# Performance work log

Hardware: AMD Instinct MI355X
Metric: run time of the kernel (lower is better)

## Reference

```python
import jax, jax.numpy as jnp
import numpy as np
from functools import partial

EPS = 1e-5
TAU = 0.1

def bn(x, g, b, axes):
    m = jnp.mean(x, axis=axes, keepdims=True)
    v = jnp.var(x, axis=axes, keepdims=True)
    return (x - m) * jax.lax.rsqrt(v + EPS) * g + b

def conv(x, w, b):
    # x: NCHW, w: OIHW, stride 1, padding 1
    y = jax.lax.conv_general_dilated(x, w, (1, 1), ((1, 1), (1, 1)),
                                     dimension_numbers=('NCHW', 'OIHW', 'NCHW'))
    return y + b[None, :, None, None]

def maxpool2(x):
    return jax.lax.reduce_window(x, -jnp.inf, jax.lax.max, (1, 1, 2, 2), (1, 1, 2, 2), 'VALID')

def setup_inputs() -> dict:
    key = jax.random.key(0)
    ks = jax.random.split(key, 24)
    s = 0.02
    B = 4096
    d = {}
    d['input_data'] = jax.random.normal(ks[0], (B, 3, 32, 32), jnp.float32)
    d['conv1_w'] = jax.random.normal(ks[1], (32, 3, 3, 3), jnp.float32) * s
    d['conv1_b'] = jnp.zeros((32,), jnp.float32)
    d['bn1_g'] = jnp.ones((32,), jnp.float32); d['bn1_b'] = jnp.zeros((32,), jnp.float32)
    d['conv2_w'] = jax.random.normal(ks[2], (64, 32, 3, 3), jnp.float32) * s
    d['conv2_b'] = jnp.zeros((64,), jnp.float32)
    d['bn2_g'] = jnp.ones((64,), jnp.float32); d['bn2_b'] = jnp.zeros((64,), jnp.float32)
    d['conv3_w'] = jax.random.normal(ks[3], (128, 64, 3, 3), jnp.float32) * s
    d['conv3_b'] = jnp.zeros((128,), jnp.float32)
    d['bn3_g'] = jnp.ones((128,), jnp.float32); d['bn3_b'] = jnp.zeros((128,), jnp.float32)
    d['pre_w'] = jax.random.normal(ks[4], (1024, 8192), jnp.float32) * s
    d['pre_b'] = jnp.zeros((1024,), jnp.float32)
    d['bnp_g'] = jnp.ones((1024,), jnp.float32); d['bnp_b'] = jnp.zeros((1024,), jnp.float32)
    d['disc_w'] = jax.random.normal(ks[5], (384, 1024), jnp.float32) * s
    d['disc_b'] = jnp.zeros((384,), jnp.float32)
    d['bnd_g'] = jnp.ones((384,), jnp.float32); d['bnd_b'] = jnp.zeros((384,), jnp.float32)
    d['dfc_w'] = jax.random.normal(ks[6], (2, 384), jnp.float32) * s
    d['dfc_b'] = jnp.zeros((2,), jnp.float32)
    d['sw_w'] = jax.random.normal(ks[7], (2, 384), jnp.float32) * s
    d['sw_b'] = jnp.zeros((2,), jnp.float32)
    # partitioned classifier: P=2, Linear(1024 -> 192) + ReLU + Linear(192 -> 10)
    d['p1_w'] = jax.random.normal(ks[8], (2, 192, 1024), jnp.float32) * s
    d['p1_b'] = jnp.zeros((2, 192), jnp.float32)
    d['p2_w'] = jax.random.normal(ks[9], (2, 10, 192), jnp.float32) * s
    d['p2_b'] = jnp.zeros((2, 10), jnp.float32)
    return d

def reference(input_data, conv1_w, conv1_b, bn1_g, bn1_b, conv2_w, conv2_b, bn2_g, bn2_b,
              conv3_w, conv3_b, bn3_g, bn3_b, pre_w, pre_b, bnp_g, bnp_b,
              disc_w, disc_b, bnd_g, bnd_b, dfc_w, dfc_b, sw_w, sw_b,
              p1_w, p1_b, p2_w, p2_b):
    B = input_data.shape[0]
    # feature extractor
    x = jax.nn.relu(bn(conv(input_data, conv1_w, conv1_b), bn1_g[None, :, None, None], bn1_b[None, :, None, None], (0, 2, 3)))
    x = maxpool2(x)
    x = jax.nn.relu(bn(conv(x, conv2_w, conv2_b), bn2_g[None, :, None, None], bn2_b[None, :, None, None], (0, 2, 3)))
    x = maxpool2(x)
    x = jax.nn.relu(bn(conv(x, conv3_w, conv3_b), bn3_g[None, :, None, None], bn3_b[None, :, None, None], (0, 2, 3)))
    feat = x.reshape(B, -1)  # [B, 8192]
    feat = jax.nn.relu(bn(feat @ pre_w.T + pre_b, bnp_g[None, :], bnp_b[None, :], (0,)))  # [B, 1024]
    # discriminator branch
    dpen = jax.nn.relu(bn(feat @ disc_w.T + disc_b, bnd_g[None, :], bnd_b[None, :], (0,)))  # [B, 384]
    domain_output = dpen @ dfc_w.T + dfc_b  # [B, 2]
    sw_logits = dpen @ sw_w.T + sw_b  # [B, P]
    # gumbel-softmax (soft) + multinomial sample of partition
    key = jax.random.key(42)
    k1, k2 = jax.random.split(key)
    u = jax.random.uniform(k1, sw_logits.shape, jnp.float32, 1e-10, 1.0)
    gumbel = -jnp.log(-jnp.log(u))
    y = jax.nn.softmax((sw_logits + gumbel) / TAU, axis=-1)  # [B, P]
    partition_idx = jax.random.categorical(k2, jnp.log(y + 1e-20), axis=-1)  # [B]
    # per-partition expert MLP computed densely (P=2), then gather chosen partition
    h = jax.nn.relu(jnp.einsum('bi,poi->pbo', feat, p1_w) + p1_b[:, None, :])  # [P, B, 192]
    logits = jnp.einsum('pbo,pco->pbc', h, p2_w) + p2_b[:, None, :]  # [P, B, 10]
    sel = logits[partition_idx, jnp.arange(B)]  # [B, 10]
    # original multiplies single-element stack by full gumbel vector and sums -> scale by sum(y)=1
    class_output_partitioned = sel * jnp.sum(y, axis=1, keepdims=True)
    return (class_output_partitioned, domain_output, partition_idx)
```

## Files before the change

### kernel.cpp

```cpp
#include <hip/hip_runtime.h>
#include <cstdint>
#include <cstddef>

typedef __attribute__((ext_vector_type(8))) short short8;
typedef __attribute__((ext_vector_type(4))) float f32x4;

__host__ __device__ inline void threefry2x32(uint32_t k0, uint32_t k1,
                                             uint32_t x0, uint32_t x1,
                                             uint32_t& o0, uint32_t& o1) {
  uint32_t ks2 = k0 ^ k1 ^ 0x1BD11BDAu;
  uint32_t v0 = x0 + k0, v1 = x1 + k1;
#define TF_R(r) { v0 += v1; v1 = (v1 << (r)) | (v1 >> (32 - (r))); v1 ^= v0; }
  TF_R(13) TF_R(15) TF_R(26) TF_R(6)
  v0 += k1; v1 += ks2 + 1u;
  TF_R(17) TF_R(29) TF_R(16) TF_R(24)
  v0 += ks2; v1 += k0 + 2u;
  TF_R(13) TF_R(15) TF_R(26) TF_R(6)
  v0 += k0; v1 += k1 + 3u;
  TF_R(17) TF_R(29) TF_R(16) TF_R(24)
  v0 += k1; v1 += ks2 + 4u;
  TF_R(13) TF_R(15) TF_R(26) TF_R(6)
  v0 += ks2; v1 += k0 + 5u;
#undef TF_R
  o0 = v0; o1 = v1;
}

__device__ __forceinline__ uint32_t tf_bits32(uint32_t k0, uint32_t k1, uint32_t j) {
  uint32_t o0, o1;
  threefry2x32(k0, k1, 0u, j, o0, o1);
  return o0 ^ o1;
}

__device__ __forceinline__ float u01_from_bits(uint32_t bits) {
  return __uint_as_float((bits >> 9) | 0x3f800000u) - 1.0f;
}

__device__ __forceinline__ float waveSum(float v) {
#pragma unroll
  for (int off = 32; off > 0; off >>= 1) v += __shfl_down(v, off, 64);
  return v;
}

__global__ __launch_bounds__(256) void conv1_fused_kernel(
    const float* __restrict__ in, const float* __restrict__ w,
    float* __restrict__ outraw, float* __restrict__ partials) {
  __shared__ float ins[3 * 34 * 34];
  __shared__ float red[4][64];
  const int b = blockIdx.x, t = threadIdx.x;
  for (int i = t; i < 3 * 34 * 34; i += 256) {
    int ci = i / 1156, r = i % 1156, iy = r / 34, ix = r % 34;
    int y = iy - 1, x = ix - 1;
    float v = 0.f;
    if ((unsigned)y < 32u && (unsigned)x < 32u)
      v = in[(((size_t)b * 3 + ci) * 32 + y) * 32 + x];
    ins[i] = v;
  }
  __syncthreads();
  const int py = t >> 4, px = t & 15, wv = t >> 6, ln = t & 63;
  float win[3][4][4];
#pragma unroll
  for (int ci = 0; ci < 3; ci++)
#pragma unroll
    for (int r = 0; r < 4; r++)
#pragma unroll
      for (int c = 0; c < 4; c++)
        win[ci][r][c] = ins[ci * 1156 + (2 * py + r) * 34 + (2 * px + c)];
#pragma unroll 1
  for (int co = 0; co < 32; co++) {
    float acc00 = 0.f, acc01 = 0.f, acc10 = 0.f, acc11 = 0.f;
#pragma unroll
    for (int ci = 0; ci < 3; ci++) {
      const float* wp = w + (co * 3 + ci) * 9;
#pragma unroll
      for (int dy = 0; dy < 3; dy++)
#pragma unroll
        for (int dx = 0; dx < 3; dx++) {
          float wvv = wp[dy * 3 + dx];
          acc00 += win[ci][dy][dx] * wvv;
          acc01 += win[ci][dy][dx + 1] * wvv;
          acc10 += win[ci][dy + 1][dx] * wvv;
          acc11 += win[ci][dy + 1][dx + 1] * wvv;
        }
    }
    float sm = acc00 + acc01 + acc10 + acc11;
    float sq = acc00 * acc00 + acc01 * acc01 + acc10 * acc10 + acc11 * acc11;
    float s = waveSum(sm), q = waveSum(sq);
    if (ln == 0) { red[wv][2 * co] = s; red[wv][2 * co + 1] = q; }
    float m = fmaxf(fmaxf(acc00, acc01), fmaxf(acc10, acc11));
    outraw[(((size_t)b * 32 + co) * 16 + py) * 16 + px] = m;
  }
  __syncthreads();
  for (int i = t; i < 64; i += 256)
    partials[(size_t)b * 64 + i] = red[0][i] + red[1][i] + red[2][i] + red[3][i];
}

__device__ __forceinline__ uint32_t pack_bf16q(float x) {
  uint32_t u = __float_as_uint(x);
  uint32_t hi = (u + 0x7fffu + ((u >> 16) & 1u)) & 0xffff0000u;
  float r = x - __uint_as_float(hi);
  uint32_t v = __float_as_uint(r);
  uint32_t lo = (v + 0x7fffu + ((v >> 16) & 1u)) >> 16;
  return hi | lo;
}

__global__ void cvt_bf16q_kernel(const float* X, uint32_t* Y, int n4) {
  int i = blockIdx.x * blockDim.x + threadIdx.x;
  if (i >= n4) return;
  float4 x = ((const float4*)X)[i];
  uint4 o;
  o.x = pack_bf16q(x.x); o.y = pack_bf16q(x.y);
  o.z = pack_bf16q(x.z); o.w = pack_bf16q(x.w);
  ((uint4*)Y)[i] = o;
}

__global__ void prep_w2_kernel(const float* __restrict__ w, short* __restrict__ wh,
                               short* __restrict__ wl) {
  int idx = blockIdx.x * 256 + threadIdx.x;
  if (idx >= 64 * 32 * 9) return;
  int tp = idx % 9, rem = idx / 9;
  int ci = rem % 32, co = rem / 32;
  uint32_t pq = pack_bf16q(w[idx]);
  size_t o = ((size_t)tp * 64 + co) * 32 + ci;
  wh[o] = (short)(pq >> 16);
  wl[o] = (short)(pq & 0xffffu);
}

__global__ void prep_w3_kernel(const float* __restrict__ w, short* __restrict__ wh,
                               short* __restrict__ wl) {
  int idx = blockIdx.x * 256 + threadIdx.x;
  if (idx >= 128 * 64 * 9) return;
  int tp = idx % 9, rem = idx / 9;
  int ci = rem % 64, co = rem / 64;
  uint32_t pq = pack_bf16q(w[idx]);
  size_t o = ((size_t)tp * 128 + co) * 64 + ci;
  wh[o] = (short)(pq >> 16);
  wl[o] = (short)(pq & 0xffffu);
}

__global__ __launch_bounds__(256) void conv2_mfma_kernel(
    const uint32_t* __restrict__ inq, const short* __restrict__ wh,
    const short* __restrict__ wl, float* __restrict__ outpool,
    float* __restrict__ partials) {
  __shared__ short Xh[324 * 32], Xl[324 * 32];
  __shared__ float red[4][128];
  const int b = blockIdx.x, t = threadIdx.x;
  for (int i = t; i < 324 * 16; i += 256) {
    int row = i >> 4;
    int py = row / 18, pxx = row % 18;
    if (py == 0 || py == 17 || pxx == 0 || pxx == 17) {
      ((uint32_t*)Xh)[i] = 0u;
      ((uint32_t*)Xl)[i] = 0u;
    }
  }
  for (int i = t; i < 4096; i += 256) {
    int p = i >> 8, px = i & 255;
    int y = px >> 4, x = px & 15;
    uint32_t ua = inq[((size_t)b * 32 + 2 * p) * 256 + px];
    uint32_t ub = inq[((size_t)b * 32 + 2 * p + 1) * 256 + px];
    uint32_t h = (ua >> 16) | (ub & 0xffff0000u);
    uint32_t l = (ua & 0xffffu) | (ub << 16);
    int row = (y + 1) * 18 + (x + 1);
    int ci2 = (2 * p) ^ ((row & 3) << 3);
    ((uint32_t*)Xh)[(row * 32 + ci2) >> 1] = h;
    ((uint32_t*)Xl)[(row * 32 + ci2) >> 1] = l;
  }
  __syncthreads();
  const int w = t >> 6, l = t & 63;
  const int lr = l & 15, lg = l >> 4;
  f32x4 acc[4][4];
#pragma unroll
  for (int i = 0; i < 4; i++)
#pragma unroll
    for (int j = 0; j < 4; j++) acc[i][j] = (f32x4){0.f, 0.f, 0.f, 0.f};
#pragma unroll 1
  for (int tap = 0; tap < 9; tap++) {
    const int dy = tap / 3, dx = tap % 3;
    short8 awh[4], awl[4];
#pragma unroll
    for (int i = 0; i < 4; i++) {
      size_t off = ((size_t)tap * 64 + i * 16 + lr) * 32 + lg * 8;
      awh[i] = *(const short8*)(wh + off);
      awl[i] = *(const short8*)(wl + off);
    }
    short8 bxh[4], bxl[4];
#pragma unroll
    for (int j = 0; j < 4; j++) {
      int y = w * 4 + j, x = lr;
      int row = (y + dy) * 18 + (x + dx);
      int ci = (lg * 8) ^ ((row & 3) << 3);
      bxh[j] = *(const short8*)&Xh[row * 32 + ci];
      bxl[j] = *(const short8*)&Xl[row * 32 + ci];
    }
#pragma unroll
    for (int i = 0; i < 4; i++)
#pragma unroll
      for (int j = 0; j < 4; j++) {
        acc[i][j] = __builtin_amdgcn_mfma_f32_16x16x32_bf16(awh[i], bxh[j], acc[i][j], 0, 0, 0);
        acc[i][j] = __builtin_amdgcn_mfma_f32_16x16x32_bf16(awh[i], bxl[j], acc[i][j], 0, 0, 0);
        acc[i][j] = __builtin_amdgcn_mfma_f32_16x16x32_bf16(awl[i], bxh[j], acc[i][j], 0, 0, 0);
      }
  }
#pragma unroll
  for (int i = 0; i < 4; i++)
#pragma unroll
    for (int r = 0; r < 4; r++) {
      int co = i * 16 + lg * 4 + r;
      float v0 = acc[i][0][r], v1 = acc[i][1][r], v2 = acc[i][2][r], v3 = acc[i][3][r];
      float s = v0 + v1 + v2 + v3;
      float q = v0 * v0 + v1 * v1 + v2 * v2 + v3 * v3;
#pragma unroll
      for (int off = 1; off <= 8; off <<= 1) {
        s += __shfl_xor(s, off, 64);
        q += __shfl_xor(q, off, 64);
      }
      if (lr == 0) { red[w][2 * co] = s; red[w][2 * co + 1] = q; }
      float h0 = fmaxf(v0, __shfl_xor(v0, 1, 64));
      float h1 = fmaxf(v1, __shfl_xor(v1, 1, 64));
      float h2 = fmaxf(v2, __shfl_xor(v2, 1, 64));
      float h3 = fmaxf(v3, __shfl_xor(v3, 1, 64));
      float pm0 = fmaxf(h0, h1);
      float pm1 = fmaxf(h2, h3);
      if ((lr & 1) == 0) {
        size_t base = ((size_t)b * 64 + co) * 64 + (w * 2) * 8 + (lr >> 1);
        outpool[base] = pm0;
        outpool[base + 8] = pm1;
      }
    }
  __syncthreads();
  for (int i = t; i < 128; i += 256)
    partials[(size_t)b * 128 + i] = red[0][i] + red[1][i] + red[2][i] + red[3][i];
}

__global__ __launch_bounds__(256) void conv3_mfma_kernel(
    const uint32_t* __restrict__ inq, const short* __restrict__ wh,
    const short* __restrict__ wl, float* __restrict__ outraw,
    float* __restrict__ partials) {
  __shared__ short Xh[100 * 64], Xl[100 * 64];
  __shared__ float red[256];
  const int b = blockIdx.x, t = threadIdx.x;
  for (int i = t; i < 100 * 32; i += 256) {
    int row = i >> 5;
    int py = row / 10, pxx = row % 10;
    if (py == 0 || py == 9 || pxx == 0 || pxx == 9) {
      ((uint32_t*)Xh)[i] = 0u;
      ((uint32_t*)Xl)[i] = 0u;
    }
  }
  for (int i = t; i < 2048; i += 256) {
    int p = i >> 6, px = i & 63;
    int y = px >> 3, x = px & 7;
    uint32_t ua = inq[((size_t)b * 64 + 2 * p) * 64 + px];
    uint32_t ub = inq[((size_t)b * 64 + 2 * p + 1) * 64 + px];
    uint32_t h = (ua >> 16) | (ub & 0xffff0000u);
    uint32_t l = (ua & 0xffffu) | (ub << 16);
    int row = (y + 1) * 10 + (x + 1);
    int ci2 = (2 * p) ^ ((row & 7) << 3);
    ((uint32_t*)Xh)[(row * 64 + ci2) >> 1] = h;
    ((uint32_t*)Xl)[(row * 64 + ci2) >> 1] = l;
  }
  __syncthreads();
  const int w = t >> 6, l = t & 63;
  const int lr = l & 15, lg = l >> 4;
  const int co_base = w * 32;
  f32x4 acc[2][4];
#pragma unroll
  for (int i = 0; i < 2; i++)
#pragma unroll
    for (int j = 0; j < 4; j++) acc[i][j] = (f32x4){0.f, 0.f, 0.f, 0.f};
#pragma unroll 1
  for (int tap = 0; tap < 9; tap++) {
    const int dy = tap / 3, dx = tap % 3;
#pragma unroll
    for (int sl = 0; sl < 2; sl++) {
      short8 awh[2], awl[2];
#pragma unroll
      for (int i = 0; i < 2; i++) {
        size_t off = ((size_t)tap * 128 + co_base + i * 16 + lr) * 64 + sl * 32 + lg * 8;
        awh[i] = *(const short8*)(wh + off);
        awl[i] = *(const short8*)(wl + off);
      }
      short8 bxh[4], bxl[4];
#pragma unroll
      for (int j = 0; j < 4; j++) {
        int px = j * 16 + lr;
        int row = ((px >> 3) + dy) * 10 + (px & 7) + dx;
        int ci = (sl * 32 + lg * 8) ^ ((row & 7) << 3);
        bxh[j] = *(const short8*)&Xh[row * 64 + ci];
        bxl[j] = *(const short8*)&Xl[row * 64 + ci];
      }
#pragma unroll
      for (int i = 0; i < 2; i++)
#pragma unroll
        for (int j = 0; j < 4; j++) {
          acc[i][j] = __builtin_amdgcn_mfma_f32_16x16x32_bf16(awh[i], bxh[j], acc[i][j], 0, 0, 0);
          acc[i][j] = __builtin_amdgcn_mfma_f32_16x16x32_bf16(awh[i], bxl[j], acc[i][j], 0, 0, 0);
          acc[i][j] = __builtin_amdgcn_mfma_f32_16x16x32_bf16(awl[i], bxh[j], acc[i][j], 0, 0, 0);
        }
    }
  }
#pragma unroll
  for (int i = 0; i < 2; i++)
#pragma unroll
    for (int r = 0; r < 4; r++) {
      int co = co_base + i * 16 + lg * 4 + r;
      float s = 0.f, q = 0.f;
#pragma unroll
      for (int j = 0; j < 4; j++) {
        float v = acc[i][j][r];
        outraw[((size_t)b * 128 + co) * 64 + j * 16 + lr] = v;
        s += v; q += v * v;
      }
#pragma unroll
      for (int off = 1; off <= 8; off <<= 1) {
        s += __shfl_xor(s, off, 64);
        q += __shfl_xor(q, off, 64);
      }
      if (lr == 0) { red[2 * co] = s; red[2 * co + 1] = q; }
    }
  __syncthreads();
  for (int i = t; i < 256; i += 256) partials[(size_t)b * 256 + i] = red[i];
}

__global__ __launch_bounds__(256) void reduce_partials_kernel(
    const float* __restrict__ partials, int nblk, int Q, double* __restrict__ sums) {
  int q = blockIdx.x;
  double acc = 0.0;
  for (int i = threadIdx.x; i < nblk; i += 256) acc += (double)partials[(size_t)i * Q + q];
  __shared__ double red[256];
  red[threadIdx.x] = acc;
  __syncthreads();
  for (int s = 128; s > 0; s >>= 1) {
    if (threadIdx.x < s) red[threadIdx.x] += red[threadIdx.x + s];
    __syncthreads();
  }
  if (threadIdx.x == 0) sums[q] = red[0];
}

__global__ __launch_bounds__(1024) void col_stats_kernel(
    const float* __restrict__ X, int R, int C, int nch, double* __restrict__ sums) {
  int c0 = blockIdx.x * 64, chunk = blockIdx.y;
  int cl = threadIdx.x & 63, rg = threadIdx.x >> 6;
  int rows = R / nch, rbeg = chunk * rows, rend = rbeg + rows;
  double s = 0.0, sq = 0.0;
  for (int r = rbeg + rg; r < rend; r += 16) {
    float v = X[(size_t)r * C + c0 + cl];
    s += v; sq += (double)v * (double)v;
  }
  __shared__ double red[16][64][2];
  red[rg][cl][0] = s; red[rg][cl][1] = sq;
  __syncthreads();
  if (rg == 0) {
    for (int i = 1; i < 16; i++) { s += red[i][cl][0]; sq += red[i][cl][1]; }
    sums[(size_t)chunk * 2 * C + 2 * (c0 + cl)] = s;
    sums[(size_t)chunk * 2 * C + 2 * (c0 + cl) + 1] = sq;
  }
}

__global__ void bn_finalize_kernel(const double* __restrict__ sums, int nch, int cst2,
                                   const float* __restrict__ g, const float* __restrict__ b,
                                   float* __restrict__ scale, float* __restrict__ shift,
                                   int C, double invN) {
  int c = blockIdx.x * blockDim.x + threadIdx.x;
  if (c >= C) return;
  double s = 0.0, sq = 0.0;
  for (int ch = 0; ch < nch; ch++) {
    s += sums[(size_t)ch * cst2 + 2 * c];
    sq += sums[(size_t)ch * cst2 + 2 * c + 1];
  }
  double m = s * invN;
  double v = sq * invN - m * m;
  double sc = (double)g[c] / sqrt(v + 1e-5);
  scale[c] = (float)sc;
  shift[c] = (float)((double)b[c] - m * sc);
}

template <int LOGHW, int CMASK>
__global__ void bn_relu_pack_vec4_kernel(float* __restrict__ X,
                                         const float* __restrict__ scale,
                                         const float* __restrict__ shift, int n4) {
  int i = blockIdx.x * blockDim.x + threadIdx.x;
  if (i >= n4) return;
  int c = ((i << 2) >> LOGHW) & CMASK;
  float4 v = ((float4*)X)[i];
  float sc = scale[c], sh = shift[c];
  uint4 o;
  o.x = pack_bf16q(fmaxf(v.x * sc + sh, 0.f));
  o.y = pack_bf16q(fmaxf(v.y * sc + sh, 0.f));
  o.z = pack_bf16q(fmaxf(v.z * sc + sh, 0.f));
  o.w = pack_bf16q(fmaxf(v.w * sc + sh, 0.f));
  ((uint4*)X)[i] = o;
}

__global__ void bn_relu_pack_cols4_kernel(float* __restrict__ X,
                                          const float* __restrict__ scale,
                                          const float* __restrict__ shift,
                                          int n4, int C4) {
  int i = blockIdx.x * blockDim.x + threadIdx.x;
  if (i >= n4) return;
  int c4 = i % C4;
  float4 v = ((float4*)X)[i];
  float4 sc = ((const float4*)scale)[c4];
  float4 sh = ((const float4*)shift)[c4];
  uint4 o;
  o.x = pack_bf16q(fmaxf(v.x * sc.x + sh.x, 0.f));
  o.y = pack_bf16q(fmaxf(v.y * sc.y + sh.y, 0.f));
  o.z = pack_bf16q(fmaxf(v.z * sc.z + sh.z, 0.f));
  o.w = pack_bf16q(fmaxf(v.w * sc.w + sh.w, 0.f));
  ((uint4*)X)[i] = o;
}

__global__ void bn_relu_cols4_kernel(float* __restrict__ X, const float* __restrict__ scale,
                                     const float* __restrict__ shift, int n4, int C4) {
  int i = blockIdx.x * blockDim.x + threadIdx.x;
  if (i >= n4) return;
  int c4 = i % C4;
  float4 v = ((float4*)X)[i];
  float4 sc = ((const float4*)scale)[c4];
  float4 sh = ((const float4*)shift)[c4];
  v.x = fmaxf(v.x * sc.x + sh.x, 0.f);
  v.y = fmaxf(v.y * sc.y + sh.y, 0.f);
  v.z = fmaxf(v.z * sc.z + sh.z, 0.f);
  v.w = fmaxf(v.w * sc.w + sh.w, 0.f);
  ((float4*)X)[i] = v;
}

template <int BIASRELU>
__global__ __launch_bounds__(256) void gemm_bf16q_kernel(
    const uint32_t* __restrict__ A, const uint32_t* __restrict__ B,
    const float* __restrict__ bias, float* __restrict__ C, int M, int N, int K) {
  __shared__ short Ah[128 * 32], Al[128 * 32], Bh[64 * 32], Bl[64 * 32];
  const int t = threadIdx.x;
  const int nTN = N >> 6;
  const int mPer = (M >> 7) >> 3;
  const int bid = blockIdx.x;
  const int xcd = bid & 7, qq = bid >> 3;
  const int m0 = (xcd * mPer + qq / nTN) << 7;
  const int n0 = (qq % nTN) << 6;
  const int w = t >> 6, l = t & 63;
  const int wrow = (w >> 1) << 6, wcol = (w & 1) << 5;
  const int lr = l & 15, lg = l >> 4;
  const int ar = t >> 1, akh = (t & 1) << 4;
  const int br = t >> 2, bkh = (t & 3) << 3;
  const int asw = (ar & 3) << 3, bsw = (br & 3) << 3;
  const uint32_t* Ap = A + (size_t)(m0 + ar) * K + akh;
  const uint32_t* Bp = B + (size_t)(n0 + br) * K + bkh;
  f32x4 acc[4][2];
#pragma unroll
  for (int i = 0; i < 4; i++)
#pragma unroll
    for (int j = 0; j < 2; j++) acc[i][j] = (f32x4){0.f, 0.f, 0.f, 0.f};
  uint4 ra0 = *(const uint4*)(Ap + 0), ra1 = *(const uint4*)(Ap + 4);
  uint4 ra2 = *(const uint4*)(Ap + 8), ra3 = *(const uint4*)(Ap + 12);
  uint4 rb0 = *(const uint4*)(Bp + 0), rb1 = *(const uint4*)(Bp + 4);
  const int NS = K >> 5;
  for (int s = 0; s < NS; s++) {
    __syncthreads();
#define STORE_G(ARR_H, ARR_L, ROW, KB, SW, U)                                   \
    {                                                                           \
      uint32_t h0 = (U.x >> 16) | (U.y & 0xffff0000u);                          \
      uint32_t h1 = (U.z >> 16) | (U.w & 0xffff0000u);                          \
      uint32_t l0 = (U.x & 0xffffu) | (U.y << 16);                              \
      uint32_t l1 = (U.z & 0xffffu) | (U.w << 16);                              \
      int idx = (ROW) * 32 + ((KB) ^ (SW));                                     \
      *(uint2*)&ARR_H[idx] = make_uint2(h0, h1);                                \
      *(uint2*)&ARR_L[idx] = make_uint2(l0, l1);                                \
    }
    STORE_G(Ah, Al, ar, akh + 0, asw, ra0)
    STORE_G(Ah, Al, ar, akh + 4, asw, ra1)
    STORE_G(Ah, Al, ar, akh + 8, asw, ra2)
    STORE_G(Ah, Al, ar, akh + 12, asw, ra3)
    STORE_G(Bh, Bl, br, bkh + 0, bsw, rb0)
    STORE_G(Bh, Bl, br, bkh + 4, bsw, rb1)
#undef STORE_G
    __syncthreads();
    if (s + 1 < NS) {
      int ko = (s + 1) << 5;
      ra0 = *(const uint4*)(Ap + ko); ra1 = *(const uint4*)(Ap + ko + 4);
      ra2 = *(const uint4*)(Ap + ko + 8); ra3 = *(const uint4*)(Ap + ko + 12);
      rb0 = *(const uint4*)(Bp + ko); rb1 = *(const uint4*)(Bp + ko + 4);
    }
    short8 ahf[4], alf[4], bhf[2], blf[2];
#pragma unroll
    for (int i = 0; i < 4; i++) {
      int R = wrow + i * 16 + lr;
      int kk = (lg << 3) ^ ((R & 3) << 3);
      ahf[i] = *(const short8*)&Ah[R * 32 + kk];
      alf[i] = *(const short8*)&Al[R * 32 + kk];
    }
#pragma unroll
    for (int j = 0; j < 2; j++) {
      int Cc = wcol + j * 16 + lr;
      int kk = (lg << 3) ^ ((Cc & 3) << 3);
      bhf[j] = *(const short8*)&Bh[Cc * 32 + kk];
      blf[j] = *(const short8*)&Bl[Cc * 32 + kk];
    }
#pragma unroll
    for (int i = 0; i < 4; i++)
#pragma unroll
      for (int j = 0; j < 2; j++) {
        acc[i][j] = __builtin_amdgcn_mfma_f32_16x16x32_bf16(ahf[i], bhf[j], acc[i][j], 0, 0, 0);
        acc[i][j] = __builtin_amdgcn_mfma_f32_16x16x32_bf16(ahf[i], blf[j], acc[i][j], 0, 0, 0);
        acc[i][j] = __builtin_amdgcn_mfma_f32_16x16x32_bf16(alf[i], bhf[j], acc[i][j], 0, 0, 0);
      }
  }
#pragma unroll
  for (int i = 0; i < 4; i++)
#pragma unroll
    for (int j = 0; j < 2; j++) {
      int n = n0 + wcol + j * 16 + lr;
#pragma unroll
      for (int r = 0; r < 4; r++) {
        int m = m0 + wrow + i * 16 + lg * 4 + r;
        float v = acc[i][j][r];
        if (BIASRELU) v = fmaxf(v + bias[n], 0.f);
        C[(size_t)m * N + n] = v;
      }
    }
}

__global__ __launch_bounds__(256) void heads_kernel(
    const float* __restrict__ dpen, const float* __restrict__ dfc_w,
    const float* __restrict__ dfc_b, const float* __restrict__ sw_w,
    const float* __restrict__ sw_b, float* __restrict__ out_dom,
    float* __restrict__ swbuf) {
  int t = blockIdx.x * 256 + threadIdx.x;
  int b = t >> 2, j = t & 3;
  const float* row = dpen + (size_t)b * 384;
  const float* wr = (j < 2) ? (dfc_w + j * 384) : (sw_w + (j - 2) * 384);
  double s = 0.0;
  for (int k = 0; k < 384; k++) s += (double)row[k] * (double)wr[k];
  s += (double)((j < 2) ? dfc_b[j] : sw_b[j - 2]);
  if (j < 2) out_dom[b * 2 + j] = (float)s;
  else swbuf[b * 2 + (j - 2)] = (float)s;
}

__global__ __launch_bounds__(256) void partition_kernel(
    const float* __restrict__ swbuf, float* __restrict__ out_pid,
    int* __restrict__ pidxI, float* __restrict__ ysum,
    uint32_t k1a, uint32_t k1b, uint32_t k2a, uint32_t k2b) {
  int b = blockIdx.x * 256 + threadIdx.x;
  if (b >= 4096) return;
  uint32_t j0 = (uint32_t)(2 * b), j1 = (uint32_t)(2 * b + 1);
  float f0 = u01_from_bits(tf_bits32(k1a, k1b, j0));
  float f1 = u01_from_bits(tf_bits32(k1a, k1b, j1));
  const float MINV = 1e-10f;
  float u0 = fmaxf(MINV, f0 * (1.0f - MINV) + MINV);
  float u1 = fmaxf(MINV, f1 * (1.0f - MINV) + MINV);
  double g0 = -log(-log((double)u0));
  double g1 = -log(-log((double)u1));
  double s0 = (double)swbuf[2 * b], s1 = (double)swbuf[2 * b + 1];
  double x0 = (s0 + g0) / 0.1;
  double x1 = (s1 + g1) / 0.1;
  double mx = fmax(x0, x1);
  double e0 = exp(x0 - mx), e1 = exp(x1 - mx);
  double es = e0 + e1;
  double y0 = e0 / es, y1 = e1 / es;
  float h0 = u01_from_bits(tf_bits32(k2a, k2b, j0));
  float h1 = u01_from_bits(tf_bits32(k2a, k2b, j1));
  const float TINY = 1.17549435e-38f;
  float v0 = fmaxf(TINY, h0 * (1.0f - TINY) + TINY);
  float v1 = fmaxf(TINY, h1 * (1.0f - TINY) + TINY);
  double gg0 = -log(-log((double)v0));
  double gg1 = -log(-log((double)v1));
  double l0 = log(y0 + 1e-20) + gg0;
  double l1 = log(y1 + 1e-20) + gg1;
  int p = (l1 > l0) ? 1 : 0;
  out_pid[b] = (float)p;
  pidxI[b] = p;
  ysum[b] = (float)(y0 + y1);
}

__global__ __launch_bounds__(256) void final_kernel(
    const float* __restrict__ h, const float* __restrict__ p2w,
    const float* __restrict__ p2b, const int* __restrict__ pidxI,
    const float* __restrict__ ysum, float* __restrict__ out0) {
  int t = blockIdx.x * 256 + threadIdx.x;
  if (t >= 40960) return;
  int b = t / 10, c = t % 10;
  int p = pidxI[b];
  const float* hr = h + (size_t)b * 384 + p * 192;
  const float* wr = p2w + ((size_t)p * 10 + c) * 192;
  float s = 0.f;
  for (int o = 0; o < 192; o++) s += hr[o] * wr[o];
  s += p2b[p * 10 + c];
  out0[t] = s * ysum[b];
}

extern "C" void kernel_launch(void* const* d_in, const int* in_sizes, int n_in,
                              void* d_out, int out_size, void* d_ws, size_t ws_size,
                              hipStream_t stream) {
  const float* input   = (const float*)d_in[0];
  const float* conv1_w = (const float*)d_in[1];
  const float* bn1_g   = (const float*)d_in[3];
  const float* bn1_b   = (const float*)d_in[4];
  const float* conv2_w = (const float*)d_in[5];
  const float* bn2_g   = (const float*)d_in[7];
  const float* bn2_b   = (const float*)d_in[8];
  const float* conv3_w = (const float*)d_in[9];
  const float* bn3_g   = (const float*)d_in[11];
  const float* bn3_b   = (const float*)d_in[12];
  const float* pre_w   = (const float*)d_in[13];
  const float* bnp_g   = (const float*)d_in[15];
  const float* bnp_b   = (const float*)d_in[16];
  const float* disc_w  = (const float*)d_in[17];
  const float* bnd_g   = (const float*)d_in[19];
  const float* bnd_b   = (const float*)d_in[20];
  const float* dfc_w   = (const float*)d_in[21];
  const float* dfc_b   = (const float*)d_in[22];
  const float* sw_w    = (const float*)d_in[23];
  const float* sw_b    = (const float*)d_in[24];
  const float* p1_w    = (const float*)d_in[25];
  const float* p1_b    = (const float*)d_in[26];
  const float* p2_w    = (const float*)d_in[27];
  const float* p2_b    = (const float*)d_in[28];

  float* W = (float*)d_ws;
  float* pool1  = W + 0;
  uint32_t* pool1q = (uint32_t*)pool1;
  float* pool2  = W + 33554432;
  uint32_t* pool2q = (uint32_t*)pool2;
  float* act3   = W + 0;
  uint32_t* Acvt = (uint32_t*)(W + 0);
  uint32_t* Bcvt = (uint32_t*)(W + 33554432);
  uint32_t* discq = (uint32_t*)(W + 41943040);
  uint32_t* p1q   = (uint32_t*)(W + 42336256);
  float* featp  = W + 50331648;
  uint32_t* featq = (uint32_t*)featp;
  short* wh3    = (short*)(W + 50331648);
  short* wl3    = (short*)(W + 50368512);
  short* wh2    = (short*)(W + 50405376);
  short* wl2    = (short*)(W + 50414592);
  float* dpen   = W + 54525952;
  float* hbuf   = W + 56098816;
  float* swbuf  = W + 57671680;
  float* ysum   = W + 57679872;
  int*   pidxI  = (int*)(W + 57683968);
  float* part   = W + 57688064;
  double* sums  = (double*)(W + 58736640);
  float* scale  = W + 58769408;
  float* shift  = W + 58770432;

  float* out_cls = (float*)d_out;
  float* out_dom = out_cls + 40960;
  float* out_pid = out_cls + 49152;

  uint32_t k1a, k1b, k2a, k2b;
  threefry2x32(0u, 42u, 0u, 0u, k1a, k1b);
  threefry2x32(0u, 42u, 0u, 1u, k2a, k2b);

  conv1_fused_kernel<<<dim3(4096), dim3(256), 0, stream>>>(input, conv1_w, pool1, part);
  reduce_partials_kernel<<<dim3(64), dim3(256), 0, stream>>>(part, 4096, 64, sums);
  bn_finalize_kernel<<<dim3(1), dim3(64), 0, stream>>>(sums, 1, 0, bn1_g, bn1_b, scale, shift, 32, 1.0 / (4096.0 * 1024.0));
  bn_relu_pack_vec4_kernel<8, 31><<<dim3(32768), dim3(256), 0, stream>>>(pool1, scale, shift, 8388608);

  prep_w2_kernel<<<dim3(72), dim3(256), 0, stream>>>(conv2_w, wh2, wl2);
  conv2_mfma_kernel<<<dim3(4096), dim3(256), 0, stream>>>(pool1q, wh2, wl2, pool2, part);
  reduce_partials_kernel<<<dim3(128), dim3(256), 0, stream>>>(part, 4096, 128, sums);
  bn_finalize_kernel<<<dim3(1), dim3(64), 0, stream>>>(sums, 1, 0, bn2_g, bn2_b, scale, shift, 64, 1.0 / (4096.0 * 256.0));
  bn_relu_pack_vec4_kernel<6, 63><<<dim3(16384), dim3(256), 0, stream>>>(pool2, scale, shift, 4194304);

  prep_w3_kernel<<<dim3(288), dim3(256), 0, stream>>>(conv3_w, wh3, wl3);
  conv3_mfma_kernel<<<dim3(4096), dim3(256), 0, stream>>>(pool2q, wh3, wl3, act3, part);
  reduce_partials_kernel<<<dim3(256), dim3(256), 0, stream>>>(part, 4096, 256, sums);
  bn_finalize_kernel<<<dim3(1), dim3(128), 0, stream>>>(sums, 1, 0, bn3_g, bn3_b, scale, shift, 128, 1.0 / (4096.0 * 64.0));
  bn_relu_pack_vec4_kernel<6, 127><<<dim3(32768), dim3(256), 0, stream>>>(act3, scale, shift, 8388608);

  cvt_bf16q_kernel<<<dim3(8192), dim3(256), 0, stream>>>(pre_w, Bcvt, 2097152);
  gemm_bf16q_kernel<0><<<dim3(512), dim3(256), 0, stream>>>(Acvt, Bcvt, (const float*)nullptr, featp, 4096, 1024, 8192);
  col_stats_kernel<<<dim3(16, 8), dim3(1024), 0, stream>>>(featp, 4096, 1024, 8, sums);
  bn_finalize_kernel<<<dim3(4), dim3(256), 0, stream>>>(sums, 8, 2048, bnp_g, bnp_b, scale, shift, 1024, 1.0 / 4096.0);
  bn_relu_pack_cols4_kernel<<<dim3(4096), dim3(256), 0, stream>>>(featp, scale, shift, 1048576, 256);

  cvt_bf16q_kernel<<<dim3(384), dim3(256), 0, stream>>>(disc_w, discq, 98304);
  cvt_bf16q_kernel<<<dim3(384), dim3(256), 0, stream>>>(p1_w, p1q, 98304);
  gemm_bf16q_kernel<0><<<dim3(192), dim3(256), 0, stream>>>(featq, discq, (const float*)nullptr, dpen, 4096, 384, 1024);
  col_stats_kernel<<<dim3(6, 8), dim3(1024), 0, stream>>>(dpen, 4096, 384, 8, sums);
  bn_finalize_kernel<<<dim3(2), dim3(256), 0, stream>>>(sums, 8, 768, bnd_g, bnd_b, scale, shift, 384, 1.0 / 4096.0);
  bn_relu_cols4_kernel<<<dim3(1536), dim3(256), 0, stream>>>(dpen, scale, shift, 393216, 96);

  heads_kernel<<<dim3(64), dim3(256), 0, stream>>>(dpen, dfc_w, dfc_b, sw_w, sw_b, out_dom, swbuf);
  partition_kernel<<<dim3(16), dim3(256), 0, stream>>>(swbuf, out_pid, pidxI, ysum, k1a, k1b, k2a, k2b);

  gemm_bf16q_kernel<1><<<dim3(192), dim3(256), 0, stream>>>(featq, p1q, p1_b, hbuf, 4096, 384, 1024);
  final_kernel<<<dim3(160), dim3(256), 0, stream>>>(hbuf, p2_w, p2_b, pidxI, ysum, out_cls);
}
```

Measured before the change: 1.026 ms.

## Use 128x128 tile GEMM kernel for the large pre-feature matmul

Adds a dedicated bf16 split-precision GEMM kernel with 128x128 block tiles and 64x64 per-wave tiles, and uses it for the 4096x1024x8192 pre-layer matmul instead of the 128x64 tile kernel. The larger tile raises arithmetic intensity per shared-memory load and halves the number of blocks. In exchange it uses more registers and shared memory, and launching 256 blocks on a 256-CU device leaves one block per CU with little latency hiding.

```diff
diff --git a/kernel.cpp b/kernel.cpp
--- a/kernel.cpp
+++ b/kernel.cpp
@@ -453,8 +453,6 @@
   uint4 ra2 = *(const uint4*)(Ap + 8), ra3 = *(const uint4*)(Ap + 12);
   uint4 rb0 = *(const uint4*)(Bp + 0), rb1 = *(const uint4*)(Bp + 4);
   const int NS = K >> 5;
-  for (int s = 0; s < NS; s++) {
-    __syncthreads();
 #define STORE_G(ARR_H, ARR_L, ROW, KB, SW, U)                                   \
     {                                                                           \
       uint32_t h0 = (U.x >> 16) | (U.y & 0xffff0000u);                          \
@@ -465,13 +463,14 @@
       *(uint2*)&ARR_H[idx] = make_uint2(h0, h1);                                \
       *(uint2*)&ARR_L[idx] = make_uint2(l0, l1);                                \
     }
+  for (int s = 0; s < NS; s++) {
+    __syncthreads();
     STORE_G(Ah, Al, ar, akh + 0, asw, ra0)
     STORE_G(Ah, Al, ar, akh + 4, asw, ra1)
     STORE_G(Ah, Al, ar, akh + 8, asw, ra2)
     STORE_G(Ah, Al, ar, akh + 12, asw, ra3)
     STORE_G(Bh, Bl, br, bkh + 0, bsw, rb0)
     STORE_G(Bh, Bl, br, bkh + 4, bsw, rb1)
-#undef STORE_G
     __syncthreads();
     if (s + 1 < NS) {
       int ko = (s + 1) << 5;
@@ -514,6 +513,90 @@
         float v = acc[i][j][r];
         if (BIASRELU) v = fmaxf(v + bias[n], 0.f);
         C[(size_t)m * N + n] = v;
+      }
+    }
+}
+
+__global__ __launch_bounds__(256, 1) void gemm_bf16q_big_kernel(
+    const uint32_t* __restrict__ A, const uint32_t* __restrict__ B,
+    float* __restrict__ C, int M, int N, int K) {
+  __shared__ short Ah[128 * 32], Al[128 * 32], Bh[128 * 32], Bl[128 * 32];
+  const int t = threadIdx.x;
+  const int nTN = N >> 7;
+  const int mPer = (M >> 7) >> 3;
+  const int bid = blockIdx.x;
+  const int xcd = bid & 7, qq = bid >> 3;
+  const int m0 = (xcd * mPer + qq / nTN) << 7;
+  const int n0 = (qq % nTN) << 7;
+  const int w = t >> 6, l = t & 63;
+  const int wrow = (w & 1) << 6, wcol = (w >> 1) << 6;
+  const int lr = l & 15, lg = l >> 4;
+  const int ar = t >> 1, akh = (t & 1) << 4;
+  const int asw = (ar & 3) << 3;
+  const uint32_t* Ap = A + (size_t)(m0 + ar) * K + akh;
+  const uint32_t* Bp = B + (size_t)(n0 + ar) * K + akh;
+  f32x4 acc[4][4];
+#pragma unroll
+  for (int i = 0; i < 4; i++)
+#pragma unroll
+    for (int j = 0; j < 4; j++) acc[i][j] = (f32x4){0.f, 0.f, 0.f, 0.f};
+  uint4 ra0 = *(const uint4*)(Ap + 0), ra1 = *(const uint4*)(Ap + 4);
+  uint4 ra2 = *(const uint4*)(Ap + 8), ra3 = *(const uint4*)(Ap + 12);
+  uint4 rb0 = *(const uint4*)(Bp + 0), rb1 = *(const uint4*)(Bp + 4);
+  uint4 rb2 = *(const uint4*)(Bp + 8), rb3 = *(const uint4*)(Bp + 12);
+  const int NS = K >> 5;
+  for (int s = 0; s < NS; s++) {
+    __syncthreads();
+    STORE_G(Ah, Al, ar, akh + 0, asw, ra0)
+    STORE_G(Ah, Al, ar, akh + 4, asw, ra1)
+    STORE_G(Ah, Al, ar, akh + 8, asw, ra2)
+    STORE_G(Ah, Al, ar, akh + 12, asw, ra3)
+    STORE_G(Bh, Bl, ar, akh + 0, asw, rb0)
+    STORE_G(Bh, Bl, ar, akh + 4, asw, rb1)
+    STORE_G(Bh, Bl, ar, akh + 8, asw, rb2)
+    STORE_G(Bh, Bl, ar, akh + 12, asw, rb3)
+    __syncthreads();
+    if (s + 1 < NS) {
+      int ko = (s + 1) << 5;
+      ra0 = *(const uint4*)(Ap + ko); ra1 = *(const uint4*)(Ap + ko + 4);
+      ra2 = *(const uint4*)(Ap + ko + 8); ra3 = *(const uint4*)(Ap + ko + 12);
+      rb0 = *(const uint4*)(Bp + ko); rb1 = *(const uint4*)(Bp + ko + 4);
+      rb2 = *(const uint4*)(Bp + ko + 8); rb3 = *(const uint4*)(Bp + ko + 12);
+    }
+    short8 ahf[4], alf[4], bhf[4], blf[4];
+#pragma unroll
+    for (int i = 0; i < 4; i++) {
+      int R = wrow + i * 16 + lr;
+      int kk = (lg << 3) ^ ((R & 3) << 3);
+      ahf[i] = *(const short8*)&Ah[R * 32 + kk];
+      alf[i] = *(const short8*)&Al[R * 32 + kk];
+    }
+#pragma unroll
+    for (int j = 0; j < 4; j++) {
+      int Cc = wcol + j * 16 + lr;
+      int kk = (lg << 3) ^ ((Cc & 3) << 3);
+      bhf[j] = *(const short8*)&Bh[Cc * 32 + kk];
+      blf[j] = *(const short8*)&Bl[Cc * 32 + kk];
+    }
+#pragma unroll
+    for (int i = 0; i < 4; i++)
+#pragma unroll
+      for (int j = 0; j < 4; j++) {
+        acc[i][j] = __builtin_amdgcn_mfma_f32_16x16x32_bf16(ahf[i], bhf[j], acc[i][j], 0, 0, 0);
+        acc[i][j] = __builtin_amdgcn_mfma_f32_16x16x32_bf16(ahf[i], blf[j], acc[i][j], 0, 0, 0);
+        acc[i][j] = __builtin_amdgcn_mfma_f32_16x16x32_bf16(alf[i], bhf[j], acc[i][j], 0, 0, 0);
+      }
+  }
+#undef STORE_G
+#pragma unroll
+  for (int i = 0; i < 4; i++)
+#pragma unroll
+    for (int j = 0; j < 4; j++) {
+      int n = n0 + wcol + j * 16 + lr;
+#pragma unroll
+      for (int r = 0; r < 4; r++) {
+        int m = m0 + wrow + i * 16 + lg * 4 + r;
+        C[(size_t)m * N + n] = acc[i][j][r];
       }
     }
 }
@@ -666,7 +749,7 @@
   bn_relu_pack_vec4_kernel<6, 127><<<dim3(32768), dim3(256), 0, stream>>>(act3, scale, shift, 8388608);
 
   cvt_bf16q_kernel<<<dim3(8192), dim3(256), 0, stream>>>(pre_w, Bcvt, 2097152);
-  gemm_bf16q_kernel<0><<<dim3(512), dim3(256), 0, stream>>>(Acvt, Bcvt, (const float*)nullptr, featp, 4096, 1024, 8192);
+  gemm_bf16q_big_kernel<<<dim3(256), dim3(256), 0, stream>>>(Acvt, Bcvt, featp, 4096, 1024, 8192);
   col_stats_kernel<<<dim3(16, 8), dim3(1024), 0, stream>>>(featp, 4096, 1024, 8, sums);
   bn_finalize_kernel<<<dim3(4), dim3(256), 0, stream>>>(sums, 8, 2048, bnp_g, bnp_b, scale, shift, 1024, 1.0 / 4096.0);
   bn_relu_pack_cols4_kernel<<<dim3(4096), dim3(256), 0, stream>>>(featp, scale, shift, 1048576, 256);
```

New measurement: 1.048 ms. +2.2%, slower.
